# Optimization experiments

Measured on AMD Instinct MI355X. Metric: run time of the kernel, lower is better.

The kernel has to match this reference:

```python
import jax, jax.numpy as jnp
import numpy as np

NUM_HEADS = 8
NUM_GROUPS = 32
EPS = 1e-5

def group_norm(x, w, b):
    B, C, H, W = x.shape
    xg = x.reshape(B, NUM_GROUPS, -1)
    mean = xg.mean(axis=-1, keepdims=True)
    var = xg.var(axis=-1, keepdims=True)
    xg = (xg - mean) * jax.lax.rsqrt(var + EPS)
    return xg.reshape(B, C, H, W) * w[None, :, None, None] + b[None, :, None, None]

def setup_inputs() -> dict:
    key = jax.random.key(0)
    ks = jax.random.split(key, 3)
    B, C, H, W = 16, 512, 32, 32
    x = jax.random.normal(ks[0], (B, C, H, W), dtype=jnp.float32)
    norm_w = jnp.ones((C,), jnp.float32)
    norm_b = jnp.zeros((C,), jnp.float32)
    qkv_w = jax.random.normal(ks[1], (3 * C, C), dtype=jnp.float32) * (C ** -0.5)
    qkv_b = jnp.zeros((3 * C,), jnp.float32)
    proj_w = jax.random.normal(ks[2], (C, C), dtype=jnp.float32) * (C ** -0.5)
    proj_b = jnp.zeros((C,), jnp.float32)
    return {"x": x, "norm_w": norm_w, "norm_b": norm_b, "qkv_w": qkv_w,
            "qkv_b": qkv_b, "proj_w": proj_w, "proj_b": proj_b}

def reference(x, norm_w, norm_b, qkv_w, qkv_b, proj_w, proj_b):
    B, C, H, W = x.shape
    nh, hd = NUM_HEADS, C // NUM_HEADS
    L = H * W
    h = group_norm(x, norm_w, norm_b)
    # 1x1 conv == channel matmul
    qkv = jnp.einsum('oc,bcl->bol', qkv_w, h.reshape(B, C, L)) + qkv_b[None, :, None]
    qkv = qkv.reshape(B, 3, nh, hd, L)
    qkv = jnp.transpose(qkv, (1, 0, 2, 4, 3))  # (3, B, nh, L, hd)
    q, k, v = qkv[0], qkv[1], qkv[2]
    scale = hd ** -0.5
    attn = jax.nn.softmax(jnp.einsum('bnqd,bnkd->bnqk', q, k) * scale, axis=-1)
    h = jnp.einsum('bnqk,bnkd->bnqd', attn, v)          # (B, nh, L, hd)
    h = jnp.transpose(h, (0, 1, 3, 2)).reshape(B, C, L)  # (B, C, L)
    h = jnp.einsum('oc,bcl->bol', proj_w, h) + proj_b[None, :, None]
    return h.reshape(B, C, H, W) + x
```

## Files before the change

### kernel.cpp

```cpp
#include <hip/hip_runtime.h>

#define BATCH 16
#define CCH   512
#define LSEQ  1024
#define NH    8
#define HD    64
#define NG    32
#define CPG   16
#define EPS   1e-5f

typedef __attribute__((ext_vector_type(8))) short short8;
typedef __attribute__((ext_vector_type(4))) float f32x4;
#define MFMA __builtin_amdgcn_mfma_f32_16x16x32_bf16

__device__ inline short f2bf(float f) {
  unsigned u = __float_as_uint(f);
  u += 0x7FFFu + ((u >> 16) & 1u);
  return (short)(u >> 16);
}

__global__ __launch_bounds__(256) void cvt_kernel(const float* __restrict__ src,
                                                  short* __restrict__ dst) {
  const int i = blockIdx.x * 256 + threadIdx.x;
  const float4 v = ((const float4*)src)[i];
  short vals[4] = {f2bf(v.x), f2bf(v.y), f2bf(v.z), f2bf(v.w)};
  *(uint2*)(dst + (size_t)i * 4) = *(uint2*)vals;
}

__global__ __launch_bounds__(256) void gn_kernel(
    const float* __restrict__ x, const float* __restrict__ nw,
    const float* __restrict__ nb, short* __restrict__ hT)
{
  const int g = blockIdx.x, b = blockIdx.y;
  const size_t base = ((size_t)b * CCH + (size_t)g * CPG) * LSEQ;
  const float4* __restrict__ x4 = (const float4*)(x + base);
  const int tid = threadIdx.x;

  __shared__ short T[16][1026];
  __shared__ float red0[4], red1[4];

  float4 v[16];
  float s = 0.f, s2 = 0.f;
#pragma unroll
  for (int r = 0; r < 16; ++r) {
    v[r] = x4[tid + 256 * r];
    s  += (v[r].x + v[r].y) + (v[r].z + v[r].w);
    s2 += (v[r].x * v[r].x + v[r].y * v[r].y) + (v[r].z * v[r].z + v[r].w * v[r].w);
  }
#pragma unroll
  for (int m = 1; m < 64; m <<= 1) { s += __shfl_xor(s, m); s2 += __shfl_xor(s2, m); }
  const int wid = tid >> 6;
  if ((tid & 63) == 0) { red0[wid] = s; red1[wid] = s2; }
  __syncthreads();
  const float ts  = (red0[0] + red0[1]) + (red0[2] + red0[3]);
  const float ts2 = (red1[0] + red1[1]) + (red1[2] + red1[3]);
  const float mean = ts * (1.f / 16384.f);
  const float var  = ts2 * (1.f / 16384.f) - mean * mean;
  const float rstd = rsqrtf(var + EPS);
#pragma unroll
  for (int r = 0; r < 16; ++r) {
    const int e = tid + 256 * r;
    const int c = e >> 8, l4 = (e & 255) * 4;
    const float sc = rstd * nw[g * CPG + c];
    const float sh = nb[g * CPG + c] - mean * sc;
    T[c][l4 + 0] = f2bf(v[r].x * sc + sh);
    T[c][l4 + 1] = f2bf(v[r].y * sc + sh);
    T[c][l4 + 2] = f2bf(v[r].z * sc + sh);
    T[c][l4 + 3] = f2bf(v[r].w * sc + sh);
  }
  __syncthreads();
  short* __restrict__ outp = hT + (size_t)b * LSEQ * CCH + g * CPG;
#pragma unroll
  for (int it = 0; it < 4; ++it) {
    const int l = tid + 256 * it;
    short vals[16];
#pragma unroll
    for (int c = 0; c < 16; ++c) vals[c] = T[c][l];
    *(short8*)(outp + (size_t)l * CCH)     = *(short8*)&vals[0];
    *(short8*)(outp + (size_t)l * CCH + 8) = *(short8*)&vals[8];
  }
}

__global__ __launch_bounds__(256) void qkv_gemm(
    const short* __restrict__ Wb, const float* __restrict__ bias,
    const short* __restrict__ hT, short* __restrict__ qT,
    short* __restrict__ kT, short* __restrict__ vv)
{
  const int b = blockIdx.z, my = blockIdx.y;
  const int m0 = my * 128, n0 = blockIdx.x * 128;
  const short* __restrict__ Bsrc = hT + (size_t)b * LSEQ * CCH;

  __shared__ short smem[2 * 128 * 72];
  short (*As)[72] = (short (*)[72])smem;
  short (*Bs)[72] = (short (*)[72])(smem + 128 * 72);

  const int tid = threadIdx.x, lane = tid & 63, w = tid >> 6;
  const int wm = (w >> 1) * 64, wn = (w & 1) * 64;
  const int l15 = lane & 15, l4g = lane >> 4;
  const int srow = tid >> 3, sk8 = (tid & 7) * 8;

  const f32x4 fz = {0.f, 0.f, 0.f, 0.f};
  f32x4 acc[4][4];
#pragma unroll
  for (int i = 0; i < 4; ++i)
#pragma unroll
    for (int j = 0; j < 4; ++j) acc[i][j] = fz;

  for (int k0 = 0; k0 < CCH; k0 += 64) {
    __syncthreads();
#pragma unroll
    for (int it = 0; it < 4; ++it) {
      const int row = srow + it * 32;
      *(short8*)&As[row][sk8] = *(const short8*)(Wb + (size_t)(m0 + row) * CCH + k0 + sk8);
      *(short8*)&Bs[row][sk8] = *(const short8*)(Bsrc + (size_t)(n0 + row) * CCH + k0 + sk8);
    }
    __syncthreads();
#pragma unroll
    for (int kk = 0; kk < 2; ++kk) {
      const int ko = kk * 32 + l4g * 8;
      short8 af[4], bf[4];
#pragma unroll
      for (int i = 0; i < 4; ++i) af[i] = *(const short8*)&As[wm + i * 16 + l15][ko];
#pragma unroll
      for (int j = 0; j < 4; ++j) bf[j] = *(const short8*)&Bs[wn + j * 16 + l15][ko];
#pragma unroll
      for (int i = 0; i < 4; ++i)
#pragma unroll
        for (int j = 0; j < 4; ++j)
          acc[i][j] = MFMA(af[i], bf[j], acc[i][j], 0, 0, 0);
    }
  }

  const int region = my >> 2;
  const float scale = (region == 0) ? 0.125f : 1.0f;
  short (*CT)[136] = (short (*)[136])smem;

  __syncthreads();
#pragma unroll
  for (int i = 0; i < 4; ++i)
#pragma unroll
    for (int r = 0; r < 4; ++r) {
      const int cl = wm + i * 16 + l4g * 4 + r;
      const float bb = bias[m0 + cl];
#pragma unroll
      for (int j = 0; j < 4; ++j) {
        const int ll = wn + j * 16 + l15;
        const short bv = f2bf((acc[i][j][r] + bb) * scale);
        if (region == 2) CT[cl][ll] = bv; else CT[ll][cl] = bv;
      }
    }
  __syncthreads();
#pragma unroll
  for (int it = 0; it < 8; ++it) {
    const int f = tid + it * 256;
    const int rr = f >> 4, c8 = (f & 15) * 8;
    const short8 val = *(const short8*)&CT[rr][c8];
    if (region == 2) {
      *(short8*)(vv + (size_t)b * CCH * LSEQ + (size_t)((my & 3) * 128 + rr) * LSEQ + n0 + c8) = val;
    } else {
      short* __restrict__ dst = (region == 0) ? qT : kT;
      *(short8*)(dst + (size_t)b * LSEQ * CCH + (size_t)(n0 + rr) * CCH + (my & 3) * 128 + c8) = val;
    }
  }
}

__global__ __launch_bounds__(256) void attn_kernel(
    const short* __restrict__ qT, const short* __restrict__ kT,
    const short* __restrict__ vv, short* __restrict__ oT)
{
  const int qt = blockIdx.x, hd = blockIdx.y, b = blockIdx.z;
  const int l0 = qt * 128, h64 = hd * 64;
  const int tid = threadIdx.x, lane = tid & 63, w = tid >> 6;
  const int l15 = lane & 15, l4g = lane >> 4;
  const int wq = w * 32;

  __shared__ short Ks[64][72];
  __shared__ short Vs[64][72];
  __shared__ short Pl[128][72];

  const short* __restrict__ qb = qT + (size_t)b * LSEQ * CCH;
  const short* __restrict__ kb = kT + (size_t)b * LSEQ * CCH;
  const short* __restrict__ vb = vv + (size_t)b * CCH * LSEQ;

  short8 qf[2][2];
#pragma unroll
  for (int mf = 0; mf < 2; ++mf)
#pragma unroll
    for (int kk = 0; kk < 2; ++kk)
      qf[mf][kk] = *(const short8*)(qb + (size_t)(l0 + wq + mf * 16 + l15) * CCH + h64 + kk * 32 + l4g * 8);

  const f32x4 fz = {0.f, 0.f, 0.f, 0.f};
  f32x4 o[2][4];
  float mr[8], lr[8];
#pragma unroll
  for (int mf = 0; mf < 2; ++mf)
#pragma unroll
    for (int df = 0; df < 4; ++df) o[mf][df] = fz;
#pragma unroll
  for (int r = 0; r < 8; ++r) { mr[r] = -1.0e30f; lr[r] = 0.f; }

  const int srow = tid >> 3, sk8 = (tid & 7) * 8;

  for (int jt = 0; jt < 16; ++jt) {
    const int j0 = jt * 64;
    __syncthreads();
#pragma unroll
    for (int it = 0; it < 2; ++it) {
      const int row = srow + it * 32;
      *(short8*)&Ks[row][sk8] = *(const short8*)(kb + (size_t)(j0 + row) * CCH + h64 + sk8);
      *(short8*)&Vs[row][sk8] = *(const short8*)(vb + (size_t)(h64 + row) * LSEQ + j0 + sk8);
    }
    __syncthreads();

    f32x4 s[2][4];
#pragma unroll
    for (int mf = 0; mf < 2; ++mf)
#pragma unroll
      for (int j = 0; j < 4; ++j) s[mf][j] = fz;
#pragma unroll
    for (int kk = 0; kk < 2; ++kk) {
      const int ko = kk * 32 + l4g * 8;
      short8 kf[4];
#pragma unroll
      for (int j = 0; j < 4; ++j) kf[j] = *(const short8*)&Ks[j * 16 + l15][ko];
#pragma unroll
      for (int mf = 0; mf < 2; ++mf)
#pragma unroll
        for (int j = 0; j < 4; ++j)
          s[mf][j] = MFMA(qf[mf][kk], kf[j], s[mf][j], 0, 0, 0);
    }

#pragma unroll
    for (int mf = 0; mf < 2; ++mf)
#pragma unroll
      for (int r = 0; r < 4; ++r) {
        const int ri = mf * 4 + r;
        float mx = fmaxf(fmaxf(s[mf][0][r], s[mf][1][r]), fmaxf(s[mf][2][r], s[mf][3][r]));
#pragma unroll
        for (int msk = 1; msk < 16; msk <<= 1) mx = fmaxf(mx, __shfl_xor(mx, msk));
        const float mnew = fmaxf(mr[ri], mx);
        const float corr = __expf(mr[ri] - mnew);
        float rs = 0.f;
#pragma unroll
        for (int j = 0; j < 4; ++j) { const float p = __expf(s[mf][j][r] - mnew); s[mf][j][r] = p; rs += p; }
#pragma unroll
        for (int msk = 1; msk < 16; msk <<= 1) rs += __shfl_xor(rs, msk);
        lr[ri] = lr[ri] * corr + rs;
        mr[ri] = mnew;
#pragma unroll
        for (int j = 0; j < 4; ++j) o[mf][j][r] *= corr;
      }

#pragma unroll
    for (int mf = 0; mf < 2; ++mf)
#pragma unroll
      for (int r = 0; r < 4; ++r) {
        const int i = wq + mf * 16 + l4g * 4 + r;
        const int sw = ((i >> 2) & 3) << 4;
#pragma unroll
        for (int j = 0; j < 4; ++j) Pl[i][(j * 16 + l15) ^ sw] = f2bf(s[mf][j][r]);
      }

#pragma unroll
    for (int kk = 0; kk < 2; ++kk) {
      const int ko = kk * 32 + l4g * 8;
      short8 pf[2], vf[4];
#pragma unroll
      for (int mf = 0; mf < 2; ++mf) {
        const int i = wq + mf * 16 + l15;
        pf[mf] = *(const short8*)&Pl[i][ko ^ (((i >> 2) & 3) << 4)];
      }
#pragma unroll
      for (int df = 0; df < 4; ++df) vf[df] = *(const short8*)&Vs[df * 16 + l15][ko];
#pragma unroll
      for (int mf = 0; mf < 2; ++mf)
#pragma unroll
        for (int df = 0; df < 4; ++df)
          o[mf][df] = MFMA(pf[mf], vf[df], o[mf][df], 0, 0, 0);
    }
  }

  short* __restrict__ ob = oT + (size_t)b * LSEQ * CCH;
#pragma unroll
  for (int mf = 0; mf < 2; ++mf)
#pragma unroll
    for (int r = 0; r < 4; ++r) {
      const float inv = 1.f / lr[mf * 4 + r];
      const int gl = l0 + wq + mf * 16 + l4g * 4 + r;
#pragma unroll
      for (int df = 0; df < 4; ++df)
        ob[(size_t)gl * CCH + h64 + df * 16 + l15] = f2bf(o[mf][df][r] * inv);
    }
}

__global__ __launch_bounds__(256) void proj_gemm(
    const short* __restrict__ Wb, const float* __restrict__ bias,
    const short* __restrict__ oT, const float* __restrict__ x,
    float* __restrict__ out)
{
  const int b = blockIdx.z;
  const int m0 = blockIdx.y * 128, n0 = blockIdx.x * 128;
  const short* __restrict__ Bsrc = oT + (size_t)b * LSEQ * CCH;

  __shared__ short As[128][72];
  __shared__ short Bs[128][72];

  const int tid = threadIdx.x, lane = tid & 63, w = tid >> 6;
  const int wm = (w >> 1) * 64, wn = (w & 1) * 64;
  const int l15 = lane & 15, l4g = lane >> 4;
  const int srow = tid >> 3, sk8 = (tid & 7) * 8;

  const f32x4 fz = {0.f, 0.f, 0.f, 0.f};
  f32x4 acc[4][4];
#pragma unroll
  for (int i = 0; i < 4; ++i)
#pragma unroll
    for (int j = 0; j < 4; ++j) acc[i][j] = fz;

  for (int k0 = 0; k0 < CCH; k0 += 64) {
    __syncthreads();
#pragma unroll
    for (int it = 0; it < 4; ++it) {
      const int row = srow + it * 32;
      *(short8*)&As[row][sk8] = *(const short8*)(Wb + (size_t)(m0 + row) * CCH + k0 + sk8);
      *(short8*)&Bs[row][sk8] = *(const short8*)(Bsrc + (size_t)(n0 + row) * CCH + k0 + sk8);
    }
    __syncthreads();
#pragma unroll
    for (int kk = 0; kk < 2; ++kk) {
      const int ko = kk * 32 + l4g * 8;
      short8 af[4], bf[4];
#pragma unroll
      for (int i = 0; i < 4; ++i) af[i] = *(const short8*)&As[wm + i * 16 + l15][ko];
#pragma unroll
      for (int j = 0; j < 4; ++j) bf[j] = *(const short8*)&Bs[wn + j * 16 + l15][ko];
#pragma unroll
      for (int i = 0; i < 4; ++i)
#pragma unroll
        for (int j = 0; j < 4; ++j)
          acc[i][j] = MFMA(af[i], bf[j], acc[i][j], 0, 0, 0);
    }
  }

  const size_t obase = (size_t)b * CCH * LSEQ;
#pragma unroll
  for (int i = 0; i < 4; ++i)
#pragma unroll
    for (int r = 0; r < 4; ++r) {
      const int gm = m0 + wm + i * 16 + l4g * 4 + r;
      const float bb = bias[gm];
#pragma unroll
      for (int j = 0; j < 4; ++j) {
        const int gl = n0 + wn + j * 16 + l15;
        const size_t idx = obase + (size_t)gm * LSEQ + gl;
        out[idx] = acc[i][j][r] + bb + x[idx];
      }
    }
}

extern "C" void kernel_launch(void* const* d_in, const int* in_sizes, int n_in,
                              void* d_out, int out_size, void* d_ws, size_t ws_size,
                              hipStream_t stream)
{
  const float* x      = (const float*)d_in[0];
  const float* norm_w = (const float*)d_in[1];
  const float* norm_b = (const float*)d_in[2];
  const float* qkv_w  = (const float*)d_in[3];
  const float* qkv_b  = (const float*)d_in[4];
  const float* proj_w = (const float*)d_in[5];
  const float* proj_b = (const float*)d_in[6];
  float* out = (float*)d_out;

  char* ws = (char*)d_ws;
  short* wq16 = (short*)ws;
  short* wp16 = (short*)(ws + 1572864);
  short* hT   = (short*)(ws + 2097152);
  short* qT   = (short*)(ws + 2097152 + 16777216);
  short* kT   = (short*)(ws + 2097152 + 2 * 16777216);
  short* vv   = (short*)(ws + 2097152 + 3 * 16777216);
  short* oT   = (short*)(ws + 2097152 + 4 * 16777216);

  cvt_kernel<<<768, 256, 0, stream>>>(qkv_w, wq16);
  cvt_kernel<<<256, 256, 0, stream>>>(proj_w, wp16);
  gn_kernel<<<dim3(NG, BATCH), 256, 0, stream>>>(x, norm_w, norm_b, hT);
  qkv_gemm<<<dim3(8, 12, BATCH), 256, 0, stream>>>(wq16, qkv_b, hT, qT, kT, vv);
  attn_kernel<<<dim3(8, NH, BATCH), 256, 0, stream>>>(qT, kT, vv, oT);
  proj_gemm<<<dim3(8, 4, BATCH), 256, 0, stream>>>(wp16, proj_b, oT, x, out);
}
```

Baseline: 286.1 us.

## Compute transposed S=K·Qᵀ per wave, shrink query tile, double attention grid

The attention kernel now processes 64 queries per block (16 per wave) instead of 128 and launches twice as many blocks. Scores are computed as K·Qᵀ, so each lane holds one query column. The row max and sum then need only two cross-lane shuffles instead of per-row 16-lane butterflies. P is packed to bf16 pairs and written to a small per-wave LDS buffer, and correction factors are broadcast via shuffles. This cuts softmax shuffle overhead and raises occupancy and parallelism. In exchange, each K/V tile loaded into LDS is reused by fewer queries, roughly doubling K/V global traffic.

```diff
diff --git a/kernel.cpp b/kernel.cpp
--- a/kernel.cpp
+++ b/kernel.cpp
@@ -168,36 +168,30 @@
     const short* __restrict__ qT, const short* __restrict__ kT,
     const short* __restrict__ vv, short* __restrict__ oT)
 {
-  const int qt = blockIdx.x, hd = blockIdx.y, b = blockIdx.z;
-  const int l0 = qt * 128, h64 = hd * 64;
+  const int qt = blockIdx.x, hh = blockIdx.y, b = blockIdx.z;
+  const int l0 = qt * 64, h64 = hh * 64;
   const int tid = threadIdx.x, lane = tid & 63, w = tid >> 6;
   const int l15 = lane & 15, l4g = lane >> 4;
-  const int wq = w * 32;
+  const int wq = w * 16;
 
   __shared__ short Ks[64][72];
   __shared__ short Vs[64][72];
-  __shared__ short Pl[128][72];
+  __shared__ unsigned Pw[4][16][36];
 
   const short* __restrict__ qb = qT + (size_t)b * LSEQ * CCH;
   const short* __restrict__ kb = kT + (size_t)b * LSEQ * CCH;
   const short* __restrict__ vb = vv + (size_t)b * CCH * LSEQ;
 
-  short8 qf[2][2];
-#pragma unroll
-  for (int mf = 0; mf < 2; ++mf)
-#pragma unroll
-    for (int kk = 0; kk < 2; ++kk)
-      qf[mf][kk] = *(const short8*)(qb + (size_t)(l0 + wq + mf * 16 + l15) * CCH + h64 + kk * 32 + l4g * 8);
+  short8 qf[2];
+#pragma unroll
+  for (int kk = 0; kk < 2; ++kk)
+    qf[kk] = *(const short8*)(qb + (size_t)(l0 + wq + l15) * CCH + h64 + kk * 32 + l4g * 8);
 
   const f32x4 fz = {0.f, 0.f, 0.f, 0.f};
-  f32x4 o[2][4];
-  float mr[8], lr[8];
-#pragma unroll
-  for (int mf = 0; mf < 2; ++mf)
-#pragma unroll
-    for (int df = 0; df < 4; ++df) o[mf][df] = fz;
-#pragma unroll
-  for (int r = 0; r < 8; ++r) { mr[r] = -1.0e30f; lr[r] = 0.f; }
+  f32x4 o[4];
+#pragma unroll
+  for (int df = 0; df < 4; ++df) o[df] = fz;
+  float mr = -1.0e30f, lr = 0.f;
 
   const int srow = tid >> 3, sk8 = (tid & 7) * 8;
 
@@ -212,11 +206,9 @@
     }
     __syncthreads();
 
-    f32x4 s[2][4];
-#pragma unroll
-    for (int mf = 0; mf < 2; ++mf)
-#pragma unroll
-      for (int j = 0; j < 4; ++j) s[mf][j] = fz;
+    f32x4 s[4];
+#pragma unroll
+    for (int j = 0; j < 4; ++j) s[j] = fz;
 #pragma unroll
     for (int kk = 0; kk < 2; ++kk) {
       const int ko = kk * 32 + l4g * 8;
@@ -224,73 +216,67 @@
 #pragma unroll
       for (int j = 0; j < 4; ++j) kf[j] = *(const short8*)&Ks[j * 16 + l15][ko];
 #pragma unroll
-      for (int mf = 0; mf < 2; ++mf)
-#pragma unroll
-        for (int j = 0; j < 4; ++j)
-          s[mf][j] = MFMA(qf[mf][kk], kf[j], s[mf][j], 0, 0, 0);
-    }
-
-#pragma unroll
-    for (int mf = 0; mf < 2; ++mf)
-#pragma unroll
-      for (int r = 0; r < 4; ++r) {
-        const int ri = mf * 4 + r;
-        float mx = fmaxf(fmaxf(s[mf][0][r], s[mf][1][r]), fmaxf(s[mf][2][r], s[mf][3][r]));
-#pragma unroll
-        for (int msk = 1; msk < 16; msk <<= 1) mx = fmaxf(mx, __shfl_xor(mx, msk));
-        const float mnew = fmaxf(mr[ri], mx);
-        const float corr = __expf(mr[ri] - mnew);
-        float rs = 0.f;
-#pragma unroll
-        for (int j = 0; j < 4; ++j) { const float p = __expf(s[mf][j][r] - mnew); s[mf][j][r] = p; rs += p; }
-#pragma unroll
-        for (int msk = 1; msk < 16; msk <<= 1) rs += __shfl_xor(rs, msk);
-        lr[ri] = lr[ri] * corr + rs;
-        mr[ri] = mnew;
-#pragma unroll
-        for (int j = 0; j < 4; ++j) o[mf][j][r] *= corr;
+      for (int j = 0; j < 4; ++j) s[j] = MFMA(kf[j], qf[kk], s[j], 0, 0, 0);
+    }
+
+    float mx = s[0][0];
+#pragma unroll
+    for (int j = 0; j < 4; ++j)
+#pragma unroll
+      for (int r = 0; r < 4; ++r) mx = fmaxf(mx, s[j][r]);
+    mx = fmaxf(mx, __shfl_xor(mx, 16));
+    mx = fmaxf(mx, __shfl_xor(mx, 32));
+    const float mnew = fmaxf(mr, mx);
+    const float corr = __expf(mr - mnew);
+    mr = mnew;
+
+    float rs = 0.f;
+    unsigned pk[4][2];
+#pragma unroll
+    for (int j = 0; j < 4; ++j) {
+      float p0 = __expf(s[j][0] - mnew), p1 = __expf(s[j][1] - mnew);
+      float p2 = __expf(s[j][2] - mnew), p3 = __expf(s[j][3] - mnew);
+      rs += (p0 + p1) + (p2 + p3);
+      pk[j][0] = (unsigned)(unsigned short)f2bf(p0) | ((unsigned)(unsigned short)f2bf(p1) << 16);
+      pk[j][1] = (unsigned)(unsigned short)f2bf(p2) | ((unsigned)(unsigned short)f2bf(p3) << 16);
+    }
+    rs += __shfl_xor(rs, 16);
+    rs += __shfl_xor(rs, 32);
+    lr = lr * corr + rs;
+
+#pragma unroll
+    for (int j = 0; j < 4; ++j)
+      *(uint2*)&Pw[w][l15][j * 8 + l4g * 2] = make_uint2(pk[j][0], pk[j][1]);
+
+    float cb[4];
+#pragma unroll
+    for (int r = 0; r < 4; ++r) cb[r] = __shfl(corr, l4g * 4 + r);
+#pragma unroll
+    for (int df = 0; df < 4; ++df)
+#pragma unroll
+      for (int r = 0; r < 4; ++r) o[df][r] *= cb[r];
+
+#pragma unroll
+    for (int kk = 0; kk < 2; ++kk) {
+      const short8 pf = *(const short8*)&Pw[w][l15][kk * 16 + l4g * 4];
+      const int ko = kk * 32 + l4g * 8;
+#pragma unroll
+      for (int df = 0; df < 4; ++df) {
+        const short8 vf = *(const short8*)&Vs[df * 16 + l15][ko];
+        o[df] = MFMA(pf, vf, o[df], 0, 0, 0);
       }
-
-#pragma unroll
-    for (int mf = 0; mf < 2; ++mf)
-#pragma unroll
-      for (int r = 0; r < 4; ++r) {
-        const int i = wq + mf * 16 + l4g * 4 + r;
-        const int sw = ((i >> 2) & 3) << 4;
-#pragma unroll
-        for (int j = 0; j < 4; ++j) Pl[i][(j * 16 + l15) ^ sw] = f2bf(s[mf][j][r]);
-      }
-
-#pragma unroll
-    for (int kk = 0; kk < 2; ++kk) {
-      const int ko = kk * 32 + l4g * 8;
-      short8 pf[2], vf[4];
-#pragma unroll
-      for (int mf = 0; mf < 2; ++mf) {
-        const int i = wq + mf * 16 + l15;
-        pf[mf] = *(const short8*)&Pl[i][ko ^ (((i >> 2) & 3) << 4)];
-      }
-#pragma unroll
-      for (int df = 0; df < 4; ++df) vf[df] = *(const short8*)&Vs[df * 16 + l15][ko];
-#pragma unroll
-      for (int mf = 0; mf < 2; ++mf)
-#pragma unroll
-        for (int df = 0; df < 4; ++df)
-          o[mf][df] = MFMA(pf[mf], vf[df], o[mf][df], 0, 0, 0);
-    }
-  }
-
+    }
+  }
+
+  float lb[4];
+#pragma unroll
+  for (int r = 0; r < 4; ++r) lb[r] = 1.f / __shfl(lr, l4g * 4 + r);
   short* __restrict__ ob = oT + (size_t)b * LSEQ * CCH;
 #pragma unroll
-  for (int mf = 0; mf < 2; ++mf)
-#pragma unroll
-    for (int r = 0; r < 4; ++r) {
-      const float inv = 1.f / lr[mf * 4 + r];
-      const int gl = l0 + wq + mf * 16 + l4g * 4 + r;
-#pragma unroll
-      for (int df = 0; df < 4; ++df)
-        ob[(size_t)gl * CCH + h64 + df * 16 + l15] = f2bf(o[mf][df][r] * inv);
-    }
+  for (int df = 0; df < 4; ++df)
+#pragma unroll
+    for (int r = 0; r < 4; ++r)
+      ob[(size_t)(l0 + wq + l4g * 4 + r) * CCH + h64 + df * 16 + l15] = f2bf(o[df][r] * lb[r]);
 }
 
 __global__ __launch_bounds__(256) void proj_gemm(
@@ -384,6 +370,6 @@
   cvt_kernel<<<256, 256, 0, stream>>>(proj_w, wp16);
   gn_kernel<<<dim3(NG, BATCH), 256, 0, stream>>>(x, norm_w, norm_b, hT);
   qkv_gemm<<<dim3(8, 12, BATCH), 256, 0, stream>>>(wq16, qkv_b, hT, qT, kT, vv);
-  attn_kernel<<<dim3(8, NH, BATCH), 256, 0, stream>>>(qT, kT, vv, oT);
+  attn_kernel<<<dim3(16, NH, BATCH), 256, 0, stream>>>(qT, kT, vv, oT);
   proj_gemm<<<dim3(8, 4, BATCH), 256, 0, stream>>>(wp16, proj_b, oT, x, out);
 }
```

New measurement: 260.9 us. 1.1x faster.
